# Optimization experiments

Hardware: AMD Instinct MI355X
Metric: run time of the kernel (lower is better)

The kernel has to match this reference:

```python
import jax, jax.numpy as jnp
import numpy as np

B, H, W, C = 2, 64, 64, 1024
L = H * W
HC, WC = 32, 32
NH, DH = 16, 64
NUM_REMAIN = 1638


def setup_inputs() -> dict:
    key = jax.random.key(0)
    ks = jax.random.split(key, 8)
    s = 1.0 / np.sqrt(C)
    x = jax.random.normal(ks[0], (B, L, C), jnp.float32)
    cached_x = jax.random.normal(ks[1], (B, HC, WC, C), jnp.float32)
    W_qkv = jax.random.normal(ks[2], (3 * C, C), jnp.float32) * s
    q_bias = jnp.zeros((C,), jnp.float32)
    v_bias = jnp.zeros((C,), jnp.float32)
    W_proj = jax.random.normal(ks[3], (C, C), jnp.float32) * s
    b_proj = jnp.zeros((C,), jnp.float32)
    scale_mul_log = jnp.full((1, NH, 1, 1), np.log(4.0), jnp.float32)
    # rope cache as (cos, sin) pairs over the flat token axis, DH//2 freqs
    ang = jax.random.uniform(ks[4], (L, DH // 2), jnp.float32) * (2 * np.pi)
    rope_grid = jnp.stack([jnp.cos(ang), jnp.sin(ang)], axis=0)  # (2, L, DH//2)
    return {"x": x, "cached_x": cached_x, "W_qkv": W_qkv, "q_bias": q_bias,
            "v_bias": v_bias, "W_proj": W_proj, "b_proj": b_proj,
            "scale_mul_log": scale_mul_log, "rope_grid": rope_grid,
            "num_remain": NUM_REMAIN}


def reference(x, cached_x, W_qkv, q_bias, v_bias, W_proj, b_proj,
              scale_mul_log, rope_grid, num_remain):
    Bx, Lx, Cx = x.shape
    # --- FastVAR token merge: MSE-to-spatial-mean selection (adaptive_avg_pool2d -> mean over L)
    mean_x = jnp.mean(x, axis=1, keepdims=True)                      # (B,1,C)
    mse = jnp.sum((x - mean_x) ** 2, axis=-1)                        # (B,L)
    idx = jnp.argsort(-mse, axis=1)[:, :num_remain]                  # (B,n) descending
    bix = jnp.arange(Bx)[:, None]
    xm = x[bix, idx]                                                 # (B,n,C) merged tokens
    # --- qkv projection with (q_bias, 0, v_bias)
    bias = jnp.concatenate([q_bias, jnp.zeros_like(q_bias), v_bias])
    qkv = (xm @ W_qkv.T + bias).reshape(Bx, -1, 3, NH, DH)
    qkv = qkv.transpose(2, 0, 3, 1, 4)                               # (3,B,H,n,dh)
    q, k, v = qkv[0], qkv[1], qkv[2]
    # --- cos attention: L2-normalize q,k; head-wise learned scale on q; sdpa scale = 1
    scale_mul = jnp.exp(jnp.minimum(scale_mul_log, jnp.log(100.0)))  # (1,NH,1,1)
    def l2n(t):
        return t / jnp.maximum(jnp.linalg.norm(t, axis=-1, keepdims=True), 1e-12)
    q = l2n(q) * scale_mul
    k = l2n(k)
    # --- 2D RoPE with per-sample gathered cache at the kept-token positions
    rc = rope_grid[:, idx, :]                                        # (2,B,n,DH//2)
    r0 = rc[0][:, None, :, :]                                        # (B,1,n,DH//2)
    r1 = rc[1][:, None, :, :]
    def rope(t):
        tp = t.reshape(*t.shape[:-1], DH // 2, 2)
        t0, t1 = tp[..., 0], tp[..., 1]
        return jnp.stack([r0 * t0 - r1 * t1, r1 * t0 + r0 * t1], axis=-1).reshape(t.shape)
    q = rope(q)
    k = rope(k)
    # --- attention over merged tokens
    attn = jax.nn.softmax(jnp.einsum('bhqd,bhkd->bhqk', q, k), axis=-1)
    o = jnp.einsum('bhqk,bhkd->bhqd', attn, v)                       # (B,H,n,dh)
    o = o.transpose(0, 2, 1, 3).reshape(Bx, -1, Cx)                  # (B,n,C)
    o = o @ W_proj.T + b_proj
    up = jnp.repeat(jnp.repeat(cached_x, 2, axis=1), 2, axis=2).reshape(Bx, Lx, Cx)
    out_full = up.at[bix, idx].set(o)
    return x + out_full
```

## Files before the change

### kernel.cpp

```cpp
#include <hip/hip_runtime.h>
#include <hip/hip_bf16.h>
#include <math.h>

#define BQ   2
#define LQ   4096
#define CQ   1024
#define NHQ  16
#define DHQ  64
#define KSEL 1638
#define KPAD 1664
#define MTOT (BQ*KSEL)
#define MPAD 3328

typedef short s16x8 __attribute__((ext_vector_type(8)));
typedef float fx4   __attribute__((ext_vector_type(4)));

#define MFMA16(a,b,c) __builtin_amdgcn_mfma_f32_16x16x32_bf16(a,b,c,0,0,0)

__device__ __forceinline__ float b2f(unsigned short u) {
  union { float f; unsigned int i; } cv; cv.i = ((unsigned int)u) << 16; return cv.f;
}
__device__ __forceinline__ unsigned short f2b(float f) {
  union { float f; unsigned int i; } cv; cv.f = f;
  unsigned int x = cv.i;
  return (unsigned short)((x + 0x7fffu + ((x >> 16) & 1u)) >> 16);
}
__device__ __forceinline__ unsigned int fbits(float f) {
  union { float f; unsigned int i; } cv; cv.f = f; return cv.i;
}
__device__ __forceinline__ void async16(const void* g, void* l) {
  __builtin_amdgcn_global_load_lds((const __attribute__((address_space(1))) void*)g,
                                   (__attribute__((address_space(3))) void*)l, 16, 0, 0);
}
__device__ __forceinline__ float fexp2(float x) {
#if __has_builtin(__builtin_amdgcn_exp2f)
  return __builtin_amdgcn_exp2f(x);
#else
  return __expf(x * 0.69314718055994531f);
#endif
}

__global__ __launch_bounds__(256) void k_cvt2(const float* __restrict__ wqkv,
                                              const float* __restrict__ wproj,
                                              unsigned short* __restrict__ wqb,
                                              unsigned short* __restrict__ wpb) {
  int i = blockIdx.x * 256 + threadIdx.x;
  const float* s; unsigned short* d; int off;
  if (i < 786432) { s = wqkv;  d = wqb; off = i; }
  else            { s = wproj; d = wpb; off = i - 786432; }
  float4 v = ((const float4*)s)[off];
  ushort4 o;
  o.x = f2b(v.x); o.y = f2b(v.y); o.z = f2b(v.z); o.w = f2b(v.w);
  ((ushort4*)d)[off] = o;
}

__global__ __launch_bounds__(256) void k_mean_part(const float* __restrict__ x,
                                                   double* __restrict__ part) {
  int bid = blockIdx.x;
  int cb = bid & 3, ch = (bid >> 2) & 31, b = bid >> 7;
  int c = cb * 256 + threadIdx.x;
  const float* p = x + ((size_t)b * LQ + (size_t)ch * 128) * CQ + c;
  double s = 0.0;
  for (int r = 0; r < 128; ++r) s += (double)p[(size_t)r * CQ];
  part[((size_t)b * 32 + ch) * CQ + c] = s;
}

__global__ __launch_bounds__(256) void k_mean_reduce(const double* __restrict__ part,
                                                     double* __restrict__ mean) {
  int g = blockIdx.x * 256 + threadIdx.x;
  int b = g >> 10, c = g & 1023;
  double s = 0.0;
  for (int ch = 0; ch < 32; ++ch) s += part[((size_t)b * 32 + ch) * CQ + c];
  mean[g] = s * (1.0 / 4096.0);
}

__global__ __launch_bounds__(256) void k_mse_base(const float* __restrict__ x,
                                                  const float* __restrict__ cached,
                                                  const double* __restrict__ mean,
                                                  double* __restrict__ mse,
                                                  float* __restrict__ out,
                                                  unsigned short* __restrict__ xb) {
  int bl = blockIdx.x; int b = bl >> 12, l = bl & 4095;
  int hh = l >> 6, ww = l & 63;
  size_t xoff = ((size_t)b * LQ + l) * CQ;
  size_t uoff = (((size_t)b * 32 + (hh >> 1)) * 32 + (ww >> 1)) * CQ;
  const double* mrow = mean + (size_t)b * CQ;
  int c0 = threadIdx.x * 4;
  float4 xv = *(const float4*)(x + xoff + c0);
  float4 uv = *(const float4*)(cached + uoff + c0);
  float4 ov;
  ov.x = xv.x + uv.x; ov.y = xv.y + uv.y; ov.z = xv.z + uv.z; ov.w = xv.w + uv.w;
  *(float4*)(out + xoff + c0) = ov;
  ushort4 xo;
  xo.x = f2b(xv.x); xo.y = f2b(xv.y); xo.z = f2b(xv.z); xo.w = f2b(xv.w);
  ((ushort4*)xb)[(xoff + c0) >> 2] = xo;
  double d0 = (double)xv.x - mrow[c0];
  double d1 = (double)xv.y - mrow[c0 + 1];
  double d2 = (double)xv.z - mrow[c0 + 2];
  double d3 = (double)xv.w - mrow[c0 + 3];
  double ss = d0 * d0 + d1 * d1 + d2 * d2 + d3 * d3;
  for (int o = 1; o < 64; o <<= 1) ss += __shfl_xor(ss, o);
  __shared__ double ws4[4];
  if ((threadIdx.x & 63) == 0) ws4[threadIdx.x >> 6] = ss;
  __syncthreads();
  if (threadIdx.x == 0) mse[(size_t)b * LQ + l] = ws4[0] + ws4[1] + ws4[2] + ws4[3];
}

__global__ __launch_bounds__(1024) void k_topk(const double* __restrict__ mse,
                                               int* __restrict__ idx_sel) {
  __shared__ unsigned long long u[4096];
  __shared__ unsigned int whist[16 * 257];
  __shared__ unsigned int wtot[4];
  __shared__ unsigned long long sh_prefix;
  __shared__ int sh_rem, sh_rem2, sh_bsel, sh_cnt, sh_eqcnt;
  __shared__ int eqbuf[256];
  int b = blockIdx.x, t = threadIdx.x;
  int wv = t >> 6, laneid = t & 63;
  for (int p = 0; p < 4; ++p) {
    int i = p * 1024 + t;
    u[i] = (unsigned long long)__double_as_longlong(mse[(size_t)b * LQ + i]);
  }
  if (t == 0) { sh_prefix = 0ULL; sh_rem = KSEL; sh_cnt = 0; sh_eqcnt = 0; }
  __syncthreads();
  for (int shift = 56; shift >= 0; shift -= 8) {
    for (int z = t; z < 16 * 257; z += 1024) whist[z] = 0u;
    __syncthreads();
    unsigned long long pref = sh_prefix;
#pragma unroll
    for (int p = 0; p < 4; ++p) {
      int i = p * 1024 + t;
      unsigned long long v = u[i];
      bool cand = (shift == 56) || ((v >> ((shift + 8) & 63)) == pref);
      if (cand) atomicAdd(&whist[wv * 257 + ((unsigned int)(v >> shift) & 255u)], 1u);
    }
    __syncthreads();
    unsigned int myc = 0, mysc = 0;
    if (t < 256) {
      unsigned int s = 0;
      int bin = 255 - t;
#pragma unroll
      for (int wvi = 0; wvi < 16; ++wvi) s += whist[wvi * 257 + bin];
      myc = s;
      mysc = myc;
#pragma unroll
      for (int o = 1; o < 64; o <<= 1) {
        unsigned int v2 = __shfl_up(mysc, o);
        if (laneid >= o) mysc += v2;
      }
      if (laneid == 63) wtot[wv] = mysc;
    }
    __syncthreads();
    if (t < 256) {
      unsigned int basep = 0;
      for (int wvi = 0; wvi < wv; ++wvi) basep += wtot[wvi];
      unsigned int incl = basep + mysc;
      unsigned int excl = incl - myc;
      unsigned int rem = (unsigned int)sh_rem;
      if (excl < rem && rem <= incl) {
        sh_bsel = 255 - t;
        sh_rem2 = (int)(rem - excl);
      }
    }
    __syncthreads();
    if (t == 0) {
      sh_prefix = (sh_prefix << 8) | (unsigned long long)sh_bsel;
      sh_rem = sh_rem2;
    }
    __syncthreads();
  }
  unsigned long long T = sh_prefix;
  int rem_eq = sh_rem;
#pragma unroll
  for (int p = 0; p < 4; ++p) {
    int i = p * 1024 + t;
    unsigned long long v = u[i];
    bool win = (v > T);
    unsigned long long mask = __ballot(win);
    int total = __popcll(mask);
    int base = 0;
    if (laneid == 0 && total > 0) base = atomicAdd(&sh_cnt, total);
    base = __shfl(base, 0);
    if (win) {
      int lpos = __popcll(mask & ((1ULL << laneid) - 1ULL));
      idx_sel[b * KPAD + base + lpos] = i;
    }
    if (v == T) {
      int e = atomicAdd(&sh_eqcnt, 1);
      if (e < 256) eqbuf[e] = i;
    }
  }
  __syncthreads();
  if (t == 0) {
    int n = sh_eqcnt; if (n > 256) n = 256;
    for (int a = 1; a < n; ++a) {
      int key = eqbuf[a]; int c = a - 1;
      while (c >= 0 && eqbuf[c] > key) { eqbuf[c + 1] = eqbuf[c]; --c; }
      eqbuf[c + 1] = key;
    }
    int base = sh_cnt;
    for (int a = 0; a < rem_eq && a < n; ++a) idx_sel[b * KPAD + base + a] = eqbuf[a];
    for (int a = KSEL; a < KPAD; ++a) idx_sel[b * KPAD + a] = 0;
  }
}

template<int MODE>
__global__ __launch_bounds__(256) void k_gemm(const unsigned short* __restrict__ Asrc,
                                              const unsigned short* __restrict__ Bmat,
                                              const int* __restrict__ idx_sel,
                                              unsigned short* __restrict__ Cbf,
                                              float* __restrict__ Cf,
                                              const float* __restrict__ xin,
                                              const float* __restrict__ bproj) {
  int bm = blockIdx.x % 26, bn = blockIdx.x / 26;
  int tid = threadIdx.x;
  int w = tid >> 6, lane = tid & 63, quad = lane >> 4, l15 = lane & 15;
  int wm = w & 1, wn = w >> 1;
  __shared__ __align__(16) unsigned char sm[16384];

  const unsigned short* gA[2];
  const unsigned short* gB[2];
#pragma unroll
  for (int p = 0; p < 2; ++p) {
    int e = p * 256 + tid; int row = e >> 2, kc = e & 3;
    int m = bm * 128 + row; if (m >= MTOT) m = MTOT - 1;
    int bb = m / KSEL; int ii = m - bb * KSEL;
    const unsigned short* rp;
    if (MODE == 0) {
      int lsel = idx_sel[bb * KPAD + ii];
      rp = Asrc + ((size_t)bb * LQ + lsel) * CQ;
    } else {
      rp = Asrc + ((size_t)bb * KPAD + ii) * CQ;
    }
    gA[p] = rp + kc * 8;
    gB[p] = Bmat + (size_t)(bn * 128 + row) * CQ + kc * 8;
  }

  fx4 acc[4][4];
#pragma unroll
  for (int a = 0; a < 4; ++a)
#pragma unroll
    for (int c = 0; c < 4; ++c) acc[a][c] = (fx4){0.f, 0.f, 0.f, 0.f};

  for (int it = 0; it < 32; ++it) {
    int ke = it * 32;
    __syncthreads();
#pragma unroll
    for (int p = 0; p < 2; ++p) {
      async16(gA[p] + ke, sm + p * 4096 + w * 1024);
      async16(gB[p] + ke, sm + 8192 + p * 4096 + w * 1024);
    }
    __syncthreads();
    s16x8 af[4], bf[4];
#pragma unroll
    for (int mt = 0; mt < 4; ++mt)
      af[mt] = *(const s16x8*)(sm + ((wm * 64 + mt * 16 + l15) * 64 + quad * 16));
#pragma unroll
    for (int nt = 0; nt < 4; ++nt)
      bf[nt] = *(const s16x8*)(sm + 8192 + ((wn * 64 + nt * 16 + l15) * 64 + quad * 16));
#pragma unroll
    for (int mt = 0; mt < 4; ++mt)
#pragma unroll
      for (int nt = 0; nt < 4; ++nt)
        acc[mt][nt] = MFMA16(af[mt], bf[nt], acc[mt][nt]);
  }

#pragma unroll
  for (int mt = 0; mt < 4; ++mt)
#pragma unroll
    for (int nt = 0; nt < 4; ++nt) {
      int n = bn * 128 + wn * 64 + nt * 16 + l15;
      int mbase = bm * 128 + wm * 64 + mt * 16 + quad * 4;
      fx4 vv = acc[mt][nt];
      if (MODE == 0) {
#pragma unroll
        for (int r = 0; r < 4; ++r) {
          int m = mbase + r;
          if (m < MTOT) Cbf[(size_t)m * 3072 + n] = f2b(vv[r]);
        }
      } else {
        float bp = bproj[n];
#pragma unroll
        for (int r = 0; r < 4; ++r) {
          int m = mbase + r;
          if (m < MTOT) {
            int bb = m / KSEL; int ii = m - bb * KSEL;
            int lsel = idx_sel[bb * KPAD + ii];
            size_t off = ((size_t)bb * LQ + lsel) * CQ + n;
            Cf[off] = xin[off] + vv[r] + bp;
          }
        }
      }
    }
}

__global__ __launch_bounds__(256) void k_normrope(const unsigned short* __restrict__ qkv,
                                                  const int* __restrict__ idx_sel,
                                                  const float* __restrict__ qbias,
                                                  const float* __restrict__ vbias,
                                                  const float* __restrict__ sml,
                                                  const float* __restrict__ rope,
                                                  unsigned short* __restrict__ qo,
                                                  unsigned short* __restrict__ ko,
                                                  unsigned short* __restrict__ vt) {
  int bid = blockIdx.x;
  int tile = bid % 26; int h = (bid / 26) & 15; int b = bid / (26 * 16);
  int tid = threadIdx.x; int w = tid >> 6; int d = tid & 63;
  __shared__ unsigned short vtile[64 * 68];
  float scale = expf(fminf(sml[h], 4.6051702f)) * 1.4426950408889634f;
  float qb = qbias[h * 64 + d];
  float vb = vbias[h * 64 + d];
  for (int pass = 0; pass < 16; ++pass) {
    int il = pass * 4 + w;
    int i = tile * 64 + il;
    float vraw = 0.f;
    if (i < KSEL) {
      int lsel = idx_sel[b * KPAD + i];
      size_t base = ((size_t)(b * KSEL + i)) * 3072 + h * 64 + d;
      int tt = d >> 1;
      float r0 = rope[(size_t)lsel * 32 + tt];
      float r1 = rope[(size_t)LQ * 32 + (size_t)lsel * 32 + tt];
      float qv = b2f(qkv[base]) + qb;
      float ss = qv * qv;
      for (int o = 1; o < 64; o <<= 1) ss += __shfl_xor(ss, o);
      float qn = qv / fmaxf(sqrtf(ss), 1e-12f) * scale;
      float qp = __shfl_xor(qn, 1);
      float qr = (d & 1) ? (r1 * qp + r0 * qn) : (r0 * qn - r1 * qp);
      qo[((size_t)(b * NHQ + h) * KPAD + i) * 64 + d] = f2b(qr);
      float kv = b2f(qkv[base + 1024]);
      float ks = kv * kv;
      for (int o = 1; o < 64; o <<= 1) ks += __shfl_xor(ks, o);
      float kn = kv / fmaxf(sqrtf(ks), 1e-12f);
      float kp = __shfl_xor(kn, 1);
      float kr = (d & 1) ? (r1 * kp + r0 * kn) : (r0 * kn - r1 * kp);
      ko[((size_t)(b * NHQ + h) * KPAD + i) * 64 + d] = f2b(kr);
      vraw = b2f(qkv[base + 2048]) + vb;
    }
    vtile[d * 68 + il] = f2b(vraw);
  }
  __syncthreads();
  int row = tid >> 2, c0 = (tid & 3) * 16;
  s16x8 o0, o1;
#pragma unroll
  for (int jj = 0; jj < 8; ++jj) {
    o0[jj] = (short)vtile[row * 68 + c0 + jj];
    o1[jj] = (short)vtile[row * 68 + c0 + 8 + jj];
  }
  size_t doff = ((size_t)((b * NHQ + h) * 64 + row)) * KPAD + (size_t)tile * 64 + c0;
  *(s16x8*)(vt + doff) = o0;
  *(s16x8*)(vt + doff + 8) = o1;
}

__global__ __launch_bounds__(256, 4) void k_attn(const unsigned short* __restrict__ qb,
                                                 const unsigned short* __restrict__ kb,
                                                 const unsigned short* __restrict__ vtb,
                                                 const float* __restrict__ sml,
                                                 unsigned short* __restrict__ pO,
                                                 float* __restrict__ pl) {
  int qt = blockIdx.x; int bh = blockIdx.y; int part = blockIdx.z;
  int b = bh >> 4, h = bh & 15;
  int t0 = part * 13, t1 = t0 + 13;
  int q0 = qt * 128;
  int tid = threadIdx.x, w = tid >> 6, lane = tid & 63, quad = lane >> 4, l15 = lane & 15;
  float M = __expf(fminf(sml[h], 4.6051702f)) * 1.4426950408889634f;
  __shared__ __align__(16) unsigned short Kt[64 * 72];
  __shared__ __align__(16) unsigned short Vt[64 * 72];
  __shared__ __align__(16) unsigned short Pq[4][32 * 72];
  unsigned short* Pw = Pq[w];
  const unsigned short* qbase = qb + (size_t)(b * NHQ + h) * KPAD * 64;
  const unsigned short* kbase = kb + (size_t)(b * NHQ + h) * KPAD * 64;
  const unsigned short* vbase = vtb + (size_t)(b * NHQ + h) * 64 * KPAD;

  s16x8 qf[2][2];
#pragma unroll
  for (int qtile = 0; qtile < 2; ++qtile)
#pragma unroll
    for (int kb2 = 0; kb2 < 2; ++kb2) {
      int row = q0 + w * 32 + qtile * 16 + l15;
      qf[qtile][kb2] = *(const s16x8*)(qbase + (size_t)row * 64 + kb2 * 32 + quad * 8);
    }

  float lsum[2] = {0.f, 0.f};
  fx4 oacc[2][4];
#pragma unroll
  for (int qtile = 0; qtile < 2; ++qtile)
#pragma unroll
    for (int dt = 0; dt < 4; ++dt) oacc[qtile][dt] = (fx4){0.f, 0.f, 0.f, 0.f};

  for (int t = t0; t < t1; ++t) {
    int j0 = t * 64;
    bool tail = (j0 + 64 > KSEL);
    __syncthreads();
#pragma unroll
    for (int p = 0; p < 2; ++p) {
      int e = p * 256 + tid; int row = e >> 3, kc = e & 7;
      *(s16x8*)(Kt + row * 72 + kc * 8) =
          *(const s16x8*)(kbase + (size_t)(j0 + row) * 64 + kc * 8);
      *(s16x8*)(Vt + row * 72 + kc * 8) =
          *(const s16x8*)(vbase + (size_t)row * KPAD + j0 + kc * 8);
    }
    __syncthreads();

    fx4 sacc[2][4];
#pragma unroll
    for (int qtile = 0; qtile < 2; ++qtile)
#pragma unroll
      for (int jj = 0; jj < 4; ++jj) sacc[qtile][jj] = (fx4){0.f, 0.f, 0.f, 0.f};
#pragma unroll
    for (int jj = 0; jj < 4; ++jj) {
      int jl = jj * 16 + l15;
      s16x8 kf0 = *(const s16x8*)(Kt + jl * 72 + quad * 8);
      s16x8 kf1 = *(const s16x8*)(Kt + jl * 72 + 32 + quad * 8);
      sacc[0][jj] = MFMA16(kf0, qf[0][0], sacc[0][jj]);
      sacc[1][jj] = MFMA16(kf0, qf[1][0], sacc[1][jj]);
      sacc[0][jj] = MFMA16(kf1, qf[0][1], sacc[0][jj]);
      sacc[1][jj] = MFMA16(kf1, qf[1][1], sacc[1][jj]);
    }
#pragma unroll
    for (int qtile = 0; qtile < 2; ++qtile)
#pragma unroll
      for (int jj = 0; jj < 4; ++jj) {
        int jbase = j0 + jj * 16 + quad * 4;
        fx4 sv = sacc[qtile][jj];
        float p0 = fexp2(sv[0] - M);
        float p1 = fexp2(sv[1] - M);
        float p2 = fexp2(sv[2] - M);
        float p3 = fexp2(sv[3] - M);
        if (tail) {
          if (jbase + 0 >= KSEL) p0 = 0.f;
          if (jbase + 1 >= KSEL) p1 = 0.f;
          if (jbase + 2 >= KSEL) p2 = 0.f;
          if (jbase + 3 >= KSEL) p3 = 0.f;
        }
        lsum[qtile] += (p0 + p1) + (p2 + p3);
        unsigned int lo = (fbits(p1) & 0xffff0000u) | (fbits(p0) >> 16);
        unsigned int hi = (fbits(p3) & 0xffff0000u) | (fbits(p2) >> 16);
        *(uint2*)(Pw + (qtile * 16 + l15) * 72 + jj * 16 + quad * 4) =
            make_uint2(lo, hi);
      }
#pragma unroll
    for (int js = 0; js < 2; ++js) {
      s16x8 pf0 = *(const s16x8*)(Pw + l15 * 72 + js * 32 + quad * 8);
      s16x8 pf1 = *(const s16x8*)(Pw + (16 + l15) * 72 + js * 32 + quad * 8);
#pragma unroll
      for (int dt = 0; dt < 4; ++dt) {
        s16x8 vf = *(const s16x8*)(Vt + (dt * 16 + l15) * 72 + js * 32 + quad * 8);
        oacc[0][dt] = MFMA16(pf0, vf, oacc[0][dt]);
        oacc[1][dt] = MFMA16(pf1, vf, oacc[1][dt]);
      }
    }
  }

#pragma unroll
  for (int qtile = 0; qtile < 2; ++qtile) {
    float s = lsum[qtile];
    s += __shfl_xor(s, 16);
    s += __shfl_xor(s, 32);
    lsum[qtile] = s;
  }

  size_t pbase = (((size_t)part * 2 + b) * NHQ + h) * KPAD;
#pragma unroll
  for (int qtile = 0; qtile < 2; ++qtile) {
    int gqb = q0 + w * 32 + qtile * 16;
    if (quad == 0) pl[pbase + gqb + l15] = lsum[qtile];
  }

#pragma unroll
  for (int qtile = 0; qtile < 2; ++qtile)
#pragma unroll
    for (int dt = 0; dt < 4; ++dt)
#pragma unroll
      for (int r = 0; r < 4; ++r)
        Pw[(qtile * 16 + quad * 4 + r) * 72 + dt * 16 + l15] = f2b(oacc[qtile][dt][r]);
#pragma unroll
  for (int pass = 0; pass < 4; ++pass) {
    int row = pass * 8 + (lane >> 3), chunk = lane & 7;
    s16x8 vv = *(const s16x8*)(Pw + row * 72 + chunk * 8);
    *(s16x8*)(pO + (pbase + q0 + w * 32 + row) * 64 + chunk * 8) = vv;
  }
}

__global__ __launch_bounds__(256) void k_comb(const unsigned short* __restrict__ pO,
                                              const float* __restrict__ pl,
                                              unsigned short* __restrict__ ob) {
  size_t g = (size_t)blockIdx.x * 256 + threadIdx.x;
  int d = (int)(g & 63);
  size_t row = g >> 6;
  int gq = (int)(row % KPAD);
  int bhh = (int)(row / KPAD);
  int b = bhh >> 4, h = bhh & 15;
  float oa = b2f(pO[g]);
  float obv = b2f(pO[g + 3407872]);
  float la = pl[row], lb = pl[row + 53248];
  float o = (oa + obv) / (la + lb);
  ob[((size_t)(b * KPAD + gq)) * CQ + h * 64 + d] = f2b(o);
}

extern "C" void kernel_launch(void* const* d_in, const int* in_sizes, int n_in,
                              void* d_out, int out_size, void* d_ws, size_t ws_size,
                              hipStream_t stream) {
  const float* x      = (const float*)d_in[0];
  const float* cached = (const float*)d_in[1];
  const float* wqkv   = (const float*)d_in[2];
  const float* qbias  = (const float*)d_in[3];
  const float* vbias  = (const float*)d_in[4];
  const float* wproj  = (const float*)d_in[5];
  const float* bproj  = (const float*)d_in[6];
  const float* sml    = (const float*)d_in[7];
  const float* rope   = (const float*)d_in[8];
  float* out = (float*)d_out;
  char* ws = (char*)d_ws;

  double* meanpart        = (double*)(ws);
  double* mean            = (double*)(ws + 524288);
  double* mse             = (double*)(ws + 540672);
  int* idx_sel            = (int*)(ws + 606208);
  unsigned short* x_bf    = (unsigned short*)(ws + 619520);
  unsigned short* wqkv_bf = (unsigned short*)(ws + 17396736);
  unsigned short* qkv     = (unsigned short*)(ws + 23688192);
  unsigned short* pO      = (unsigned short*)(ws + 619520);
  float* pl               = (float*)(ws + 14251008);
  unsigned short* wproj_bf= (unsigned short*)(ws + 44135424);
  unsigned short* qo      = (unsigned short*)(ws + 46232576);
  unsigned short* ko      = (unsigned short*)(ws + 53048320);
  unsigned short* vt      = (unsigned short*)(ws + 59864064);
  unsigned short* ob      = (unsigned short*)(ws + 66679808);

  hipLaunchKernelGGL(k_cvt2, dim3(4096), dim3(256), 0, stream, wqkv, wproj,
                     wqkv_bf, wproj_bf);
  hipLaunchKernelGGL(k_mean_part, dim3(256), dim3(256), 0, stream, x, meanpart);
  hipLaunchKernelGGL(k_mean_reduce, dim3(8), dim3(256), 0, stream, meanpart, mean);
  hipLaunchKernelGGL(k_mse_base, dim3(8192), dim3(256), 0, stream, x, cached, mean, mse,
                     out, x_bf);
  hipLaunchKernelGGL(k_topk, dim3(BQ), dim3(1024), 0, stream, mse, idx_sel);
  hipLaunchKernelGGL((k_gemm<0>), dim3(26 * 24), dim3(256), 0, stream,
                     x_bf, wqkv_bf, idx_sel, qkv, (float*)nullptr,
                     (const float*)nullptr, (const float*)nullptr);
  hipLaunchKernelGGL(k_normrope, dim3(26 * 16 * BQ), dim3(256), 0, stream,
                     qkv, idx_sel, qbias, vbias, sml, rope, qo, ko, vt);
  hipLaunchKernelGGL(k_attn, dim3(13, BQ * NHQ, 2), dim3(256), 0, stream,
                     qo, ko, vt, sml, pO, pl);
  hipLaunchKernelGGL(k_comb, dim3(13312), dim3(256), 0, stream, pO, pl, ob);
  hipLaunchKernelGGL((k_gemm<1>), dim3(26 * 8), dim3(256), 0, stream,
                     ob, wproj_bf, idx_sel, (unsigned short*)nullptr, out, x, bproj);
}
```

Baseline: 309.3 us.

## Double-buffer GEMM shared-memory loads and retile output projection GEMM

Splits the templated GEMM into two kernels. Both now double-buffer the async global-to-LDS loads, so the next K tile is fetched while MFMAs run on the current one, using explicit vmcnt waits and raw barriers. The output projection GEMM switches to 64x64 tiles with K=64 per stage and a swizzled block order, raising the grid from 208 to 832 blocks so more CUs are busy. This doubles LDS per block and relies on hand-counted vmcnt values that must match the number of outstanding async loads.

```diff
diff --git a/kernel.cpp b/kernel.cpp
--- a/kernel.cpp
+++ b/kernel.cpp
@@ -203,19 +203,15 @@
   }
 }
 
-template<int MODE>
-__global__ __launch_bounds__(256) void k_gemm(const unsigned short* __restrict__ Asrc,
-                                              const unsigned short* __restrict__ Bmat,
-                                              const int* __restrict__ idx_sel,
-                                              unsigned short* __restrict__ Cbf,
-                                              float* __restrict__ Cf,
-                                              const float* __restrict__ xin,
-                                              const float* __restrict__ bproj) {
+__global__ __launch_bounds__(256) void k_gemmA(const unsigned short* __restrict__ Asrc,
+                                               const unsigned short* __restrict__ Bmat,
+                                               const int* __restrict__ idx_sel,
+                                               unsigned short* __restrict__ Cbf) {
   int bm = blockIdx.x % 26, bn = blockIdx.x / 26;
   int tid = threadIdx.x;
   int w = tid >> 6, lane = tid & 63, quad = lane >> 4, l15 = lane & 15;
   int wm = w & 1, wn = w >> 1;
-  __shared__ __align__(16) unsigned char sm[16384];
+  __shared__ __align__(16) unsigned char sm[2][16384];
 
   const unsigned short* gA[2];
   const unsigned short* gB[2];
@@ -224,14 +220,8 @@
     int e = p * 256 + tid; int row = e >> 2, kc = e & 3;
     int m = bm * 128 + row; if (m >= MTOT) m = MTOT - 1;
     int bb = m / KSEL; int ii = m - bb * KSEL;
-    const unsigned short* rp;
-    if (MODE == 0) {
-      int lsel = idx_sel[bb * KPAD + ii];
-      rp = Asrc + ((size_t)bb * LQ + lsel) * CQ;
-    } else {
-      rp = Asrc + ((size_t)bb * KPAD + ii) * CQ;
-    }
-    gA[p] = rp + kc * 8;
+    int lsel = idx_sel[bb * KPAD + ii];
+    gA[p] = Asrc + ((size_t)bb * LQ + lsel) * CQ + kc * 8;
     gB[p] = Bmat + (size_t)(bn * 128 + row) * CQ + kc * 8;
   }
 
@@ -241,28 +231,36 @@
 #pragma unroll
     for (int c = 0; c < 4; ++c) acc[a][c] = (fx4){0.f, 0.f, 0.f, 0.f};
 
+#define STAGE_A(buf, it) do { int ke = (it) * 32;                                   \
+    _Pragma("unroll")                                                               \
+    for (int p = 0; p < 2; ++p) {                                                   \
+      async16(gA[p] + ke, sm[buf] + p * 4096 + w * 1024);                           \
+      async16(gB[p] + ke, sm[buf] + 8192 + p * 4096 + w * 1024);                    \
+    } } while (0)
+
+  STAGE_A(0, 0);
   for (int it = 0; it < 32; ++it) {
-    int ke = it * 32;
-    __syncthreads();
-#pragma unroll
-    for (int p = 0; p < 2; ++p) {
-      async16(gA[p] + ke, sm + p * 4096 + w * 1024);
-      async16(gB[p] + ke, sm + 8192 + p * 4096 + w * 1024);
-    }
-    __syncthreads();
+    int cur = it & 1;
+    if (it < 31) STAGE_A(cur ^ 1, it + 1);
+    if (it < 31) asm volatile("s_waitcnt vmcnt(4)");
+    else         asm volatile("s_waitcnt vmcnt(0)");
+    __builtin_amdgcn_s_barrier();
+    const unsigned char* smb = sm[cur];
     s16x8 af[4], bf[4];
 #pragma unroll
     for (int mt = 0; mt < 4; ++mt)
-      af[mt] = *(const s16x8*)(sm + ((wm * 64 + mt * 16 + l15) * 64 + quad * 16));
+      af[mt] = *(const s16x8*)(smb + ((wm * 64 + mt * 16 + l15) * 64 + quad * 16));
 #pragma unroll
     for (int nt = 0; nt < 4; ++nt)
-      bf[nt] = *(const s16x8*)(sm + 8192 + ((wn * 64 + nt * 16 + l15) * 64 + quad * 16));
+      bf[nt] = *(const s16x8*)(smb + 8192 + ((wn * 64 + nt * 16 + l15) * 64 + quad * 16));
 #pragma unroll
     for (int mt = 0; mt < 4; ++mt)
 #pragma unroll
       for (int nt = 0; nt < 4; ++nt)
         acc[mt][nt] = MFMA16(af[mt], bf[nt], acc[mt][nt]);
-  }
+    __builtin_amdgcn_s_barrier();
+  }
+#undef STAGE_A
 
 #pragma unroll
   for (int mt = 0; mt < 4; ++mt)
@@ -271,23 +269,96 @@
       int n = bn * 128 + wn * 64 + nt * 16 + l15;
       int mbase = bm * 128 + wm * 64 + mt * 16 + quad * 4;
       fx4 vv = acc[mt][nt];
-      if (MODE == 0) {
-#pragma unroll
-        for (int r = 0; r < 4; ++r) {
-          int m = mbase + r;
-          if (m < MTOT) Cbf[(size_t)m * 3072 + n] = f2b(vv[r]);
-        }
-      } else {
-        float bp = bproj[n];
-#pragma unroll
-        for (int r = 0; r < 4; ++r) {
-          int m = mbase + r;
-          if (m < MTOT) {
-            int bb = m / KSEL; int ii = m - bb * KSEL;
-            int lsel = idx_sel[bb * KPAD + ii];
-            size_t off = ((size_t)bb * LQ + lsel) * CQ + n;
-            Cf[off] = xin[off] + vv[r] + bp;
-          }
+#pragma unroll
+      for (int r = 0; r < 4; ++r) {
+        int m = mbase + r;
+        if (m < MTOT) Cbf[(size_t)m * 3072 + n] = f2b(vv[r]);
+      }
+    }
+}
+
+__global__ __launch_bounds__(256) void k_gemmB(const unsigned short* __restrict__ Asrc,
+                                               const unsigned short* __restrict__ Bmat,
+                                               const int* __restrict__ idx_sel,
+                                               float* __restrict__ Cf,
+                                               const float* __restrict__ xin,
+                                               const float* __restrict__ bproj) {
+  int bid = blockIdx.x;
+  int swz = (bid & 7) * 104 + (bid >> 3);
+  int bm = swz % 52, bn = swz / 52;
+  int tid = threadIdx.x;
+  int w = tid >> 6, lane = tid & 63, quad = lane >> 4, l15 = lane & 15;
+  int wm = w & 1, wn = w >> 1;
+  __shared__ __align__(16) unsigned char sm[2][16384];
+
+  const unsigned short* g4[4];
+#pragma unroll
+  for (int p = 0; p < 4; ++p) {
+    int e = (p & 1) * 256 + tid; int row = e >> 3, kc = e & 7;
+    if (p < 2) {
+      int m = bm * 64 + row; if (m >= MTOT) m = MTOT - 1;
+      int bb = m / KSEL; int ii = m - bb * KSEL;
+      g4[p] = Asrc + ((size_t)bb * KPAD + ii) * CQ + kc * 8;
+    } else {
+      g4[p] = Bmat + (size_t)(bn * 64 + row) * CQ + kc * 8;
+    }
+  }
+
+  fx4 acc[2][2];
+#pragma unroll
+  for (int a = 0; a < 2; ++a)
+#pragma unroll
+    for (int c = 0; c < 2; ++c) acc[a][c] = (fx4){0.f, 0.f, 0.f, 0.f};
+
+#define STAGE_B(buf, it) do { int ke = (it) * 64;                                   \
+    _Pragma("unroll")                                                               \
+    for (int p = 0; p < 4; ++p)                                                     \
+      async16(g4[p] + ke, sm[buf] + p * 4096 + w * 1024);                           \
+    } while (0)
+
+  STAGE_B(0, 0);
+  for (int it = 0; it < 16; ++it) {
+    int cur = it & 1;
+    if (it < 15) STAGE_B(cur ^ 1, it + 1);
+    if (it < 15) asm volatile("s_waitcnt vmcnt(4)");
+    else         asm volatile("s_waitcnt vmcnt(0)");
+    __builtin_amdgcn_s_barrier();
+    const unsigned char* smb = sm[cur];
+#pragma unroll
+    for (int kk = 0; kk < 2; ++kk) {
+      s16x8 af[2], bf2[2];
+#pragma unroll
+      for (int mt = 0; mt < 2; ++mt)
+        af[mt] = *(const s16x8*)(smb + ((wm * 32 + mt * 16 + l15) * 64 + kk * 32 + quad * 8) * 2);
+#pragma unroll
+      for (int nt = 0; nt < 2; ++nt)
+        bf2[nt] = *(const s16x8*)(smb + 8192 + ((wn * 32 + nt * 16 + l15) * 64 + kk * 32 + quad * 8) * 2);
+#pragma unroll
+      for (int mt = 0; mt < 2; ++mt)
+#pragma unroll
+        for (int nt = 0; nt < 2; ++nt)
+          acc[mt][nt] = MFMA16(af[mt], bf2[nt], acc[mt][nt]);
+    }
+    __builtin_amdgcn_s_barrier();
+  }
+#undef STAGE_B
+
+#pragma unroll
+  for (int mt = 0; mt < 2; ++mt)
+#pragma unroll
+    for (int nt = 0; nt < 2; ++nt) {
+      int n = bn * 64 + wn * 32 + nt * 16 + l15;
+      int mbase = bm * 64 + wm * 32 + mt * 16 + quad * 4;
+      fx4 vv = acc[mt][nt];
+      float bp = bproj[n];
+#pragma unroll
+      for (int r = 0; r < 4; ++r) {
+        int m = mbase + r;
+        if (m < MTOT) {
+          int bb = m / KSEL; int ii = m - bb * KSEL;
+          int lsel = idx_sel[bb * KPAD + ii];
+          size_t off = ((size_t)bb * LQ + lsel) * CQ + n;
+          Cf[off] = xin[off] + vv[r] + bp;
         }
       }
     }
@@ -533,14 +604,13 @@
   hipLaunchKernelGGL(k_mse_base, dim3(8192), dim3(256), 0, stream, x, cached, mean, mse,
                      out, x_bf);
   hipLaunchKernelGGL(k_topk, dim3(BQ), dim3(1024), 0, stream, mse, idx_sel);
-  hipLaunchKernelGGL((k_gemm<0>), dim3(26 * 24), dim3(256), 0, stream,
-                     x_bf, wqkv_bf, idx_sel, qkv, (float*)nullptr,
-                     (const float*)nullptr, (const float*)nullptr);
+  hipLaunchKernelGGL(k_gemmA, dim3(26 * 24), dim3(256), 0, stream,
+                     x_bf, wqkv_bf, idx_sel, qkv);
   hipLaunchKernelGGL(k_normrope, dim3(26 * 16 * BQ), dim3(256), 0, stream,
                      qkv, idx_sel, qbias, vbias, sml, rope, qo, ko, vt);
   hipLaunchKernelGGL(k_attn, dim3(13, BQ * NHQ, 2), dim3(256), 0, stream,
                      qo, ko, vt, sml, pO, pl);
   hipLaunchKernelGGL(k_comb, dim3(13312), dim3(256), 0, stream, pO, pl, ob);
-  hipLaunchKernelGGL((k_gemm<1>), dim3(26 * 8), dim3(256), 0, stream,
-                     ob, wproj_bf, idx_sel, (unsigned short*)nullptr, out, x, bproj);
-}
+  hipLaunchKernelGGL(k_gemmB, dim3(832), dim3(256), 0, stream,
+                     ob, wproj_bf, idx_sel, out, x, bproj);
+}
```

New measurement: 285.8 us. 7.6% less time.
